# Kernel optimization log

Hardware: AMD Instinct MI355X
Metric: run time of the kernel (lower is better)

## Reference

```python
import jax, jax.numpy as jnp
import numpy as np

BETA = 0.25  # commitment loss coefficient


def setup_inputs() -> dict:
    key = jax.random.key(0)
    kx, kc = jax.random.split(key)
    # x: [B, T, D] latents; codebooks: [M, K, D] (equal K per level -> stacked)
    x = jax.random.normal(kx, (64, 1024, 256), dtype=jnp.float32)
    # small init akin to RandomUniform(-1/K, 1/K)
    codebooks = jax.random.normal(kc, (4, 1024, 256), dtype=jnp.float32) * (1.0 / 1024.0)
    return {"x": x, "codebooks": codebooks}


def reference(x, codebooks):
    """Residual VQ forward (inference path: no EMA state update).

    Returns (y, commit_loss): y = x + stop_grad(sum_l q_l - x) (straight-through),
    commit_loss = beta * sum_l mean((stop_grad(q_l) - r_l)^2).
    """
    D = x.shape[-1]
    M = codebooks.shape[0]
    flat = x.reshape(-1, D)                      # [N, D]
    residual = flat
    q_sum = jnp.zeros_like(flat)
    commit = jnp.zeros((), dtype=x.dtype)
    for lvl in range(M):                         # M is small & fixed (4)
        cb = codebooks[lvl]                      # [K, D]
        # squared L2 distances: ||r||^2 + ||e||^2 - 2 r.e^T
        r2 = jnp.sum(residual * residual, axis=1, keepdims=True)   # [N, 1]
        e2 = jnp.sum(cb * cb, axis=1)                               # [K]
        dist = r2 + e2 - 2.0 * jnp.matmul(residual, cb.T)           # [N, K]
        idx = jnp.argmin(dist, axis=1)                              # [N]
        q = jnp.take(cb, idx, axis=0)                               # [N, D]
        q_st = jax.lax.stop_gradient(q)
        commit = commit + BETA * jnp.mean((q_st - residual) ** 2)
        q_sum = q_sum + q
        residual = residual - q_st
    y_flat = flat + jax.lax.stop_gradient(q_sum - flat)
    return y_flat.reshape(x.shape), commit
```

## Files before the change

kernel.cpp:

```cpp
#include <hip/hip_runtime.h>

#define DIM 256
#define KCODES 1024
#define LEVELS 4
#define CHUNK 64
#define NCHUNK 16
#define TOKB 128
#define NTOK 65536
#define NELEM (NTOK * DIM)

typedef _Float16 h8 __attribute__((ext_vector_type(8)));
typedef _Float16 h4 __attribute__((ext_vector_type(4)));
typedef _Float16 h2 __attribute__((ext_vector_type(2)));
typedef float f4 __attribute__((ext_vector_type(4)));
typedef unsigned int u32;

__device__ __forceinline__ void gload16(const void* g, void* l) {
  __builtin_amdgcn_global_load_lds(
      (const __attribute__((address_space(1))) void*)g,
      (__attribute__((address_space(3))) void*)l, 16, 0, 0);
}

__device__ __forceinline__ float sq8(h8 r, float acc) {
#if __has_builtin(__builtin_amdgcn_fdot2)
  #pragma unroll
  for (int j = 0; j < 4; ++j) {
    h2 p = {r[2 * j], r[2 * j + 1]};
    acc = __builtin_amdgcn_fdot2(p, p, acc, false);
  }
#else
  #pragma unroll
  for (int j = 0; j < 8; ++j) { float v = (float)r[j]; acc += v * v; }
#endif
  return acc;
}


__global__ __launch_bounds__(256) void rvq_prep(const float* __restrict__ cb,
                                                _Float16* __restrict__ cb16,
                                                float* __restrict__ e2p,
                                                float* __restrict__ out) {
  if (blockIdx.x == 0 && threadIdx.x == 0) out[NELEM] = 0.0f;
  const int row = blockIdx.x * 4 + (threadIdx.x >> 6);
  const int lane = threadIdx.x & 63;
  const float* src = cb + (size_t)row * DIM + lane * 4;
  f4 v = *(const f4*)src;
  h4 hv;
  hv[0] = (_Float16)v[0]; hv[1] = (_Float16)v[1];
  hv[2] = (_Float16)v[2]; hv[3] = (_Float16)v[3];
  const int g = lane >> 1;
  char* dst = (char*)cb16 + (((size_t)row >> 6) << 15) + (((row >> 4) & 3) << 13) +
              ((g >> 2) << 10) + ((((g & 3) << 4) + (row & 15)) << 4) +
              ((lane & 1) << 3);
  *(h4*)dst = hv;
  float s = v[0]*v[0] + v[1]*v[1] + v[2]*v[2] + v[3]*v[3];
  #pragma unroll
  for (int off = 32; off; off >>= 1) s += __shfl_xor(s, off, 64);
  if (lane == 0) e2p[row] = 0.25f - 0.5f * s;
}

__global__ __launch_bounds__(256, 2) void rvq_main(
    const float* __restrict__ x, const float* __restrict__ cb32,
    const _Float16* __restrict__ cb16, const float* __restrict__ e2p,
    float* __restrict__ out) {
  __shared__ __attribute__((aligned(16))) _Float16 clds[2][CHUNK * DIM];
  __shared__ __attribute__((aligned(16))) float e2_lds[KCODES];
  __shared__ __attribute__((aligned(16))) int idx_hist[TOKB][4];
  __shared__ float r2_sh[TOKB];
  __shared__ float csum_sh[4];

  const int tid = threadIdx.x;
  const int wave = tid >> 6, lane = tid & 63;
  const int col = lane & 15, quad = lane >> 4;

  const int sl_off = wave * 8192;
  const int sg0 = sl_off + (lane << 4);
  const char* cb16b = (const char*)cb16;

  {
    const char* gsrc = cb16b + sg0;
    char* ldst = (char*)&clds[0][0] + sl_off;
    #pragma unroll
    for (int i = 0; i < 8; ++i) gload16(gsrc + i * 1024, ldst + i * 1024);
  }

  h8 af[2][8];
  float r2p[2] = {0.f, 0.f};
  const size_t tok0 = (size_t)blockIdx.x * TOKB + wave * 32;
  #pragma unroll
  for (int mt = 0; mt < 2; ++mt) {
    const float* xr = x + (tok0 + mt * 16 + col) * DIM + quad * 8;
    #pragma unroll
    for (int kk = 0; kk < 8; ++kk) {
      f4 a = *(const f4*)(xr + kk * 32);
      f4 b = *(const f4*)(xr + kk * 32 + 4);
      h8 h;
      #pragma unroll
      for (int j = 0; j < 4; ++j) { h[j] = (_Float16)a[j]; h[4 + j] = (_Float16)b[j]; }
      af[mt][kk] = h;
      r2p[mt] = sq8(h, r2p[mt]);
    }
  }

  float commit_acc = 0.f;

  for (int lvl = 0; lvl < LEVELS; ++lvl) {
    #pragma unroll
    for (int mt = 0; mt < 2; ++mt) {
      float s = r2p[mt];
      s += __shfl_xor(s, 16, 64);
      s += __shfl_xor(s, 32, 64);
      if (quad == 0) r2_sh[wave * 32 + mt * 16 + col] = s;
    }
    *(f4*)&e2_lds[tid * 4] = *(const f4*)(e2p + (lvl << 10) + tid * 4);

    u32 best[2][4];
    #pragma unroll
    for (int mt = 0; mt < 2; ++mt)
      #pragma unroll
      for (int i = 0; i < 4; ++i) best[mt][i] = 0u;

    for (int c = 0; c < NCHUNK; ++c) {
      __syncthreads();
      {
        const int gn = lvl * NCHUNK + c + 1;
        const char* gsrc = cb16b + ((size_t)(gn < 64 ? gn : 63) << 15) + sg0;
        char* ldst = (char*)&clds[(c + 1) & 1][0] + sl_off;
        #pragma unroll
        for (int i = 0; i < 8; ++i) gload16(gsrc + i * 1024, ldst + i * 1024);
      }

      const char* cbuf = (const char*)&clds[c & 1][0] + (lane << 4);
      #pragma unroll
      for (int nt = 0; nt < 4; ++nt) {
        const int code0 = c * 64 + nt * 16;
        const float e2v = e2_lds[code0 + col];
        f4 acc0 = {e2v, e2v, e2v, e2v};
        f4 acc1 = acc0;
        #pragma unroll
        for (int kk = 0; kk < 8; ++kk) {
          h8 b = *(const h8*)(cbuf + ((nt * 8 + kk) << 10));
          acc0 = __builtin_amdgcn_mfma_f32_16x16x32_f16(af[0][kk], b, acc0, 0, 0, 0);
          acc1 = __builtin_amdgcn_mfma_f32_16x16x32_f16(af[1][kk], b, acc1, 0, 0, 0);
        }
        const u32 invc = (u32)(code0 + col) ^ 1023u;
        #pragma unroll
        for (int i = 0; i < 4; ++i) {
          u32 p0 = (__float_as_uint(acc0[i]) & 0xFFFFFC00u) | invc;
          if (p0 > best[0][i]) best[0][i] = p0;
          u32 p1 = (__float_as_uint(acc1[i]) & 0xFFFFFC00u) | invc;
          if (p1 > best[1][i]) best[1][i] = p1;
        }
      }
    }

    #pragma unroll
    for (int mt = 0; mt < 2; ++mt)
      #pragma unroll
      for (int i = 0; i < 4; ++i) {
        u32 b = best[mt][i];
        #pragma unroll
        for (int off = 1; off < 16; off <<= 1) {
          u32 o = __shfl_xor(b, off, 16);
          if (o > b) b = o;
        }
        best[mt][i] = b;
      }

    if (col == 0) {
      #pragma unroll
      for (int mt = 0; mt < 2; ++mt)
        #pragma unroll
        for (int i = 0; i < 4; ++i) {
          const u32 p = best[mt][i];
          const int code = (int)((p & 1023u) ^ 1023u);
          const int t = wave * 32 + mt * 16 + quad * 4 + i;
          idx_hist[t][lvl] = code;
          const float sc = __uint_as_float(p & 0xFFFFFC00u) - 0.25f;
          commit_acc += r2_sh[t] - 2.0f * sc;
        }
    }
    __syncthreads();

    if (lvl < LEVELS - 1) {
      r2p[0] = 0.f; r2p[1] = 0.f;
      #pragma unroll
      for (int mt = 0; mt < 2; ++mt) {
        const int qidx = idx_hist[wave * 32 + mt * 16 + col][lvl];
        const int G = (lvl << 10) + qidx;
        const char* qbase = cb16b + ((size_t)(G >> 6) << 15) + (((G >> 4) & 3) << 13) +
                            ((quad * 16 + (G & 15)) << 4);
        #pragma unroll
        for (int kk = 0; kk < 8; ++kk) {
          h8 q = *(const h8*)(qbase + (kk << 10));
          h8 r = af[mt][kk] - q;
          af[mt][kk] = r;
          r2p[mt] = sq8(r, r2p[mt]);
        }
      }
    }
  }

  float* yblk = out + (size_t)blockIdx.x * (TOKB * DIM);
  #pragma unroll 4
  for (int it = 0; it < 32; ++it) {
    const int f = it * 1024 + tid * 4;
    const int t = f >> 8;
    const int d = f & 255;
    const int4 qi = *(const int4*)&idx_hist[t][0];
    f4 q0 = *(const f4*)(cb32 + (size_t)qi.x * DIM + d);
    f4 q1 = *(const f4*)(cb32 + (size_t)(1024 + qi.y) * DIM + d);
    f4 q2 = *(const f4*)(cb32 + (size_t)(2048 + qi.z) * DIM + d);
    f4 q3 = *(const f4*)(cb32 + (size_t)(3072 + qi.w) * DIM + d);
    f4 yv = (q0 + q1) + (q2 + q3);
    *(f4*)(yblk + f) = yv;
  }

  #pragma unroll
  for (int off = 1; off < 64; off <<= 1) commit_acc += __shfl_xor(commit_acc, off, 64);
  if (lane == 0) csum_sh[wave] = commit_acc;
  __syncthreads();
  if (tid == 0) {
    const float tot = csum_sh[0] + csum_sh[1] + csum_sh[2] + csum_sh[3];
    atomicAdd(out + NELEM, tot * (0.25f / 16777216.0f));
  }
}

extern "C" void kernel_launch(void* const* d_in, const int* in_sizes, int n_in,
                              void* d_out, int out_size, void* d_ws, size_t ws_size,
                              hipStream_t stream) {
  const float* x = (const float*)d_in[0];
  const float* cb = (const float*)d_in[1];
  float* out = (float*)d_out;
  _Float16* cb16 = (_Float16*)d_ws;
  float* e2p = (float*)((char*)d_ws + (size_t)LEVELS * KCODES * DIM * sizeof(_Float16));

  rvq_prep<<<(LEVELS * KCODES) / 4, 256, 0, stream>>>(cb, cb16, e2p, out);
  rvq_main<<<NTOK / TOKB, 256, 0, stream>>>(x, cb, cb16, e2p, out);
}
```

Baseline: 253.9 us.

## Halve block and codebook chunk size to raise occupancy, read e2 from global

Shrinks the main kernel to 128 threads and 64 tokens per block, and halves the codebook chunk to 32 codes. The fp16 codebook layout in the prep kernel is rewritten to match, with wider per-thread stores. The per-level e2 staging into LDS is dropped and the values are read straight from global memory. The aim is more resident blocks per CU and less LDS per block, at the cost of twice as many chunk iterations and barriers and more codebook traffic per token.

```diff
diff --git a/kernel.cpp b/kernel.cpp
--- a/kernel.cpp
+++ b/kernel.cpp
@@ -3,14 +3,13 @@
 #define DIM 256
 #define KCODES 1024
 #define LEVELS 4
-#define CHUNK 64
-#define NCHUNK 16
-#define TOKB 128
+#define CHUNK 32
+#define NCHUNK 32
+#define TOKB 64
 #define NTOK 65536
 #define NELEM (NTOK * DIM)
 
 typedef _Float16 h8 __attribute__((ext_vector_type(8)));
-typedef _Float16 h4 __attribute__((ext_vector_type(4)));
 typedef _Float16 h2 __attribute__((ext_vector_type(2)));
 typedef float f4 __attribute__((ext_vector_type(4)));
 typedef unsigned int u32;
@@ -41,33 +40,32 @@
                                                 float* __restrict__ e2p,
                                                 float* __restrict__ out) {
   if (blockIdx.x == 0 && threadIdx.x == 0) out[NELEM] = 0.0f;
-  const int row = blockIdx.x * 4 + (threadIdx.x >> 6);
-  const int lane = threadIdx.x & 63;
-  const float* src = cb + (size_t)row * DIM + lane * 4;
-  f4 v = *(const f4*)src;
-  h4 hv;
-  hv[0] = (_Float16)v[0]; hv[1] = (_Float16)v[1];
-  hv[2] = (_Float16)v[2]; hv[3] = (_Float16)v[3];
-  const int g = lane >> 1;
-  char* dst = (char*)cb16 + (((size_t)row >> 6) << 15) + (((row >> 4) & 3) << 13) +
-              ((g >> 2) << 10) + ((((g & 3) << 4) + (row & 15)) << 4) +
-              ((lane & 1) << 3);
-  *(h4*)dst = hv;
-  float s = v[0]*v[0] + v[1]*v[1] + v[2]*v[2] + v[3]*v[3];
-  #pragma unroll
-  for (int off = 32; off; off >>= 1) s += __shfl_xor(s, off, 64);
-  if (lane == 0) e2p[row] = 0.25f - 0.5f * s;
-}
-
-__global__ __launch_bounds__(256, 2) void rvq_main(
+  const int row = blockIdx.x * 8 + (threadIdx.x >> 5);
+  const int g = threadIdx.x & 31;
+  const float* src = cb + (size_t)row * DIM + g * 8;
+  f4 a = *(const f4*)src;
+  f4 b = *(const f4*)(src + 4);
+  h8 hv;
+  #pragma unroll
+  for (int j = 0; j < 4; ++j) { hv[j] = (_Float16)a[j]; hv[4 + j] = (_Float16)b[j]; }
+  char* dst = (char*)cb16 + (((size_t)row >> 5) << 14) + (((row >> 4) & 1) << 13) +
+              ((g >> 2) << 10) + ((((g & 3) << 4) + (row & 15)) << 4);
+  *(h8*)dst = hv;
+  float s = a[0]*a[0] + a[1]*a[1] + a[2]*a[2] + a[3]*a[3] +
+            b[0]*b[0] + b[1]*b[1] + b[2]*b[2] + b[3]*b[3];
+  #pragma unroll
+  for (int off = 16; off; off >>= 1) s += __shfl_xor(s, off, 32);
+  if (g == 0) e2p[row] = 0.25f - 0.5f * s;
+}
+
+__global__ __launch_bounds__(128, 4) void rvq_main(
     const float* __restrict__ x, const float* __restrict__ cb32,
     const _Float16* __restrict__ cb16, const float* __restrict__ e2p,
     float* __restrict__ out) {
   __shared__ __attribute__((aligned(16))) _Float16 clds[2][CHUNK * DIM];
-  __shared__ __attribute__((aligned(16))) float e2_lds[KCODES];
   __shared__ __attribute__((aligned(16))) int idx_hist[TOKB][4];
   __shared__ float r2_sh[TOKB];
-  __shared__ float csum_sh[4];
+  __shared__ float csum_sh[2];
 
   const int tid = threadIdx.x;
   const int wave = tid >> 6, lane = tid & 63;
@@ -112,7 +110,7 @@
       s += __shfl_xor(s, 32, 64);
       if (quad == 0) r2_sh[wave * 32 + mt * 16 + col] = s;
     }
-    *(f4*)&e2_lds[tid * 4] = *(const f4*)(e2p + (lvl << 10) + tid * 4);
+    const float* e2_lvl = e2p + (lvl << 10);
 
     u32 best[2][4];
     #pragma unroll
@@ -124,7 +122,7 @@
       __syncthreads();
       {
         const int gn = lvl * NCHUNK + c + 1;
-        const char* gsrc = cb16b + ((size_t)(gn < 64 ? gn : 63) << 15) + sg0;
+        const char* gsrc = cb16b + ((size_t)(gn < 128 ? gn : 127) << 14) + sg0;
         char* ldst = (char*)&clds[(c + 1) & 1][0] + sl_off;
         #pragma unroll
         for (int i = 0; i < 8; ++i) gload16(gsrc + i * 1024, ldst + i * 1024);
@@ -132,9 +130,9 @@
 
       const char* cbuf = (const char*)&clds[c & 1][0] + (lane << 4);
       #pragma unroll
-      for (int nt = 0; nt < 4; ++nt) {
-        const int code0 = c * 64 + nt * 16;
-        const float e2v = e2_lds[code0 + col];
+      for (int nt = 0; nt < 2; ++nt) {
+        const int code0 = c * 32 + nt * 16;
+        const float e2v = e2_lvl[code0 + col];
         f4 acc0 = {e2v, e2v, e2v, e2v};
         f4 acc1 = acc0;
         #pragma unroll
@@ -188,7 +186,7 @@
       for (int mt = 0; mt < 2; ++mt) {
         const int qidx = idx_hist[wave * 32 + mt * 16 + col][lvl];
         const int G = (lvl << 10) + qidx;
-        const char* qbase = cb16b + ((size_t)(G >> 6) << 15) + (((G >> 4) & 3) << 13) +
+        const char* qbase = cb16b + ((size_t)(G >> 5) << 14) + (((G >> 4) & 1) << 13) +
                             ((quad * 16 + (G & 15)) << 4);
         #pragma unroll
         for (int kk = 0; kk < 8; ++kk) {
@@ -204,7 +202,7 @@
   float* yblk = out + (size_t)blockIdx.x * (TOKB * DIM);
   #pragma unroll 4
   for (int it = 0; it < 32; ++it) {
-    const int f = it * 1024 + tid * 4;
+    const int f = it * 512 + tid * 4;
     const int t = f >> 8;
     const int d = f & 255;
     const int4 qi = *(const int4*)&idx_hist[t][0];
@@ -221,8 +219,7 @@
   if (lane == 0) csum_sh[wave] = commit_acc;
   __syncthreads();
   if (tid == 0) {
-    const float tot = csum_sh[0] + csum_sh[1] + csum_sh[2] + csum_sh[3];
-    atomicAdd(out + NELEM, tot * (0.25f / 16777216.0f));
+    atomicAdd(out + NELEM, (csum_sh[0] + csum_sh[1]) * (0.25f / 16777216.0f));
   }
 }
 
@@ -235,6 +232,6 @@
   _Float16* cb16 = (_Float16*)d_ws;
   float* e2p = (float*)((char*)d_ws + (size_t)LEVELS * KCODES * DIM * sizeof(_Float16));
 
-  rvq_prep<<<(LEVELS * KCODES) / 4, 256, 0, stream>>>(cb, cb16, e2p, out);
-  rvq_main<<<NTOK / TOKB, 256, 0, stream>>>(x, cb, cb16, e2p, out);
-}
+  rvq_prep<<<(LEVELS * KCODES) / 8, 256, 0, stream>>>(cb, cb16, e2p, out);
+  rvq_main<<<NTOK / TOKB, 128, 0, stream>>>(x, cb, cb16, e2p, out);
+}
```

After: 274.5 us. +8.1%, slower.
